# Performance work log

Measured on AMD Instinct MI355X. Metric: run time of the kernel, lower is better.

Reference implementation:

```python
import jax, jax.numpy as jnp
import numpy as np

NUM_LAYERS = 5  # shared parameters across layers


def _crelu(z):
    # complex ReLU: ReLU applied independently to real and imag parts
    return jnp.maximum(z.real, 0.0) + 1j * jnp.maximum(z.imag, 0.0)


def _layer(Habs2, diagH, noise, maxpow, v, ar, dl, rc):
    # ---- u step ----
    # cov: [B,K,1] = |H|^2 @ |v|^2 (sum over last dim keepdim is identity for width-1) + noise
    cov = jnp.sum(Habs2 @ (jnp.abs(v) ** 2), axis=-1, keepdims=True) + noise[..., None]
    u = diagH[..., None] * v / cov  # [B,K,1] complex
    # ---- w step ---- (w_poly=None branch)
    err = 1.0 - jnp.conj(u) * diagH[..., None] * v
    w = 1.0 / err  # [B,K,1] complex
    # ---- v step ----
    v_tilde = jnp.conj(diagH)[..., None] * u * w  # [B,K,1]
    ul = (jnp.abs(u) ** 2) * jnp.abs(w)  # real [B,K,1]
    ul = jnp.sum(jnp.abs(jnp.swapaxes(Habs2, -2, -1) @ ul), axis=-1, keepdims=True)
    mu = jnp.maximum(jnp.abs(v_tilde) / jnp.sqrt(maxpow)[..., None] - ul, 0.0)
    ula = (ul + mu).astype(v_tilde.dtype)
    # ar + diagload branches: [B,K,1,1] @ [1,C] -> [B,K,1,C]
    vt = (v_tilde / ula)[..., None] @ ar + v_tilde[..., None] @ dl
    # nonlin + recombination: [B,K,1,C] @ [C,1] -> [B,K,1,1]
    vt = _crelu(vt) @ rc
    v_new = vt[..., 0]  # [B,K,1]
    # power correction
    cur = jnp.maximum(maxpow[..., None], jnp.abs(v_new) ** 2)
    corr = jnp.minimum(jnp.sqrt(maxpow[..., None] / cur), 1.0)
    return v_new * corr, u, w


def setup_inputs() -> dict:
    key = jax.random.key(0)
    ks = jax.random.split(key, 12)
    B, K, C = 64, 512, 4
    s = 1.0 / np.sqrt(C + 1)
    inp = {
        "h_re": jax.random.normal(ks[0], (B, K, K), jnp.float32),
        "h_im": jax.random.normal(ks[1], (B, K, K), jnp.float32),
        "user_noise_pow": jax.random.uniform(ks[2], (B, K), jnp.float32, 0.1, 1.0),
        "bss_maxpow": jnp.ones((B, K), jnp.float32),
        "v_in_re": jax.random.normal(ks[3], (B, K, 1), jnp.float32) * 0.5,
        "v_in_im": jax.random.normal(ks[4], (B, K, 1), jnp.float32) * 0.5,
        "ar_re": jax.random.normal(ks[5], (1, C), jnp.float32) * s,
        "ar_im": jax.random.normal(ks[6], (1, C), jnp.float32) * s,
        "dl_re": jax.random.normal(ks[7], (1, C), jnp.float32) * s,
        "dl_im": jax.random.normal(ks[8], (1, C), jnp.float32) * s,
        "rc_re": jax.random.normal(ks[9], (C, 1), jnp.float32) * s,
        "rc_im": jax.random.normal(ks[10], (C, 1), jnp.float32) * s,
    }
    return inp


def reference(h_re, h_im, user_noise_pow, bss_maxpow, v_in_re, v_in_im,
              ar_re, ar_im, dl_re, dl_im, rc_re, rc_im):
    H = (h_re + 1j * h_im).astype(jnp.complex64)
    Habs2 = h_re * h_re + h_im * h_im  # |H|^2, real [B,K,K]
    diagH = jnp.diagonal(H, axis1=-2, axis2=-1)  # [B,K]
    v = (v_in_re + 1j * v_in_im).astype(jnp.complex64)
    ar = (ar_re + 1j * ar_im).astype(jnp.complex64)
    dl = (dl_re + 1j * dl_im).astype(jnp.complex64)
    rc = (rc_re + 1j * rc_im).astype(jnp.complex64)
    vs = []
    for _ in range(NUM_LAYERS):
        v, u, w = _layer(Habs2, diagH, user_noise_pow, bss_maxpow, v, ar, dl, rc)
        vs.append(v)
    vstack = jnp.stack(vs, 0)  # [L,B,K,1] complex
    # return real/imag stacked so the output is a real tensor: [L,B,K,1,2]
    return jnp.stack([vstack.real, vstack.imag], axis=-1)
```

## Files before the change

### kernel.cpp

```cpp
#include <hip/hip_runtime.h>

#define B    64
#define K    512
#define C    4
#define NL   5
#define BK   (B*K)
#define ROWS 128
#define NT   1024
#define GRID (B*4)

typedef _Float16 half_t;
typedef _Float16 half8 __attribute__((ext_vector_type(8)));
typedef float    f4    __attribute__((ext_vector_type(4)));

#define PART_OFF   0
#define VST_OFF    (36*K*4)
#define XSQ_OFF    (VST_OFF + K*8)
#define MPL_OFF    (XSQ_OFF + K*4)
#define NZ_OFF     (MPL_OFF + K*4)
#define DAB_OFF    (NZ_OFF + ROWS*4)
#define RSB_OFF    (DAB_OFF + ROWS*4)
#define SMEM_BYTES (RSB_OFF + ROWS*4)

__device__ __forceinline__ float ld_l3(const float* p) {
    return __uint_as_float(__hip_atomic_load((const unsigned*)p,
        __ATOMIC_RELAXED, __HIP_MEMORY_SCOPE_AGENT));
}
__device__ __forceinline__ void st_l3(float* p, float v) {
    __hip_atomic_store((unsigned*)p, __float_as_uint(v),
        __ATOMIC_RELAXED, __HIP_MEMORY_SCOPE_AGENT);
}
__device__ __forceinline__ void st_l3_2(float2* p, float2 v) {
    unsigned long long u = ((unsigned long long)__float_as_uint(v.y) << 32)
                         | (unsigned long long)__float_as_uint(v.x);
    __hip_atomic_store((unsigned long long*)p, u,
        __ATOMIC_RELAXED, __HIP_MEMORY_SCOPE_AGENT);
}
__device__ __forceinline__ float2 ld_l3_2(const float2* p) {
    unsigned long long u = __hip_atomic_load((const unsigned long long*)p,
        __ATOMIC_RELAXED, __HIP_MEMORY_SCOPE_AGENT);
    return make_float2(__uint_as_float((unsigned)(u & 0xffffffffu)),
                       __uint_as_float((unsigned)(u >> 32)));
}

__global__ __launch_bounds__(NT, 4) void k_all(
    const float* __restrict__ hre,  const float* __restrict__ him,
    const float* __restrict__ noise,const float* __restrict__ mp,
    const float* __restrict__ vre,  const float* __restrict__ vim,
    const float* __restrict__ ar_re,const float* __restrict__ ar_im,
    const float* __restrict__ dl_re,const float* __restrict__ dl_im,
    const float* __restrict__ rc_re,const float* __restrict__ rc_im,
    float2* __restrict__ vtilde,
    float*  __restrict__ ulpart,
    unsigned* __restrict__ bar,
    float* __restrict__ out)
{
    extern __shared__ char smem[];
    float*  part  = (float*) (smem + PART_OFF);
    float2* vst   = (float2*)(smem + VST_OFF);
    float*  xsq   = (float*) (smem + XSQ_OFF);
    float*  mpl   = (float*) (smem + MPL_OFF);
    float*  nz    = (float*) (smem + NZ_OFF);
    float*  dab   = (float*) (smem + DAB_OFF);
    float*  rsbuf = (float*) (smem + RSB_OFF);

    const int tid  = threadIdx.x;
    const int lane = tid & 63;
    const int w    = tid >> 6;
    const int b    = blockIdx.x & 63;
    const int q    = blockIdx.x >> 6;
    const int j0   = q * ROWS;
    unsigned* qb   = bar + ((unsigned)b << 5);

    if (tid < K) {
        float a = vre[b * K + tid], c2 = vim[b * K + tid];
        vst[tid] = make_float2(a, c2);
        xsq[tid] = a * a + c2 * c2;
        mpl[tid] = mp[b * K + tid];
    } else if (tid < K + ROWS) {
        nz[tid - K] = noise[b * K + j0 + (tid - K)];
    }
    __syncthreads();

    half8 h[8];
    {
        const f4 xa = ((const f4*)xsq)[lane * 2];
        const f4 xb = ((const f4*)xsq)[lane * 2 + 1];
        const size_t gb = ((size_t)b * K + j0) * K;
        const f4* rp = (const f4*)(hre + gb);
        const f4* ip = (const f4*)(him + gb);
        f4 lr0[2], lr1[2], li0[2], li1[2];
        lr0[0] = __builtin_nontemporal_load(rp + tid * 2);
        lr1[0] = __builtin_nontemporal_load(rp + tid * 2 + 1);
        li0[0] = __builtin_nontemporal_load(ip + tid * 2);
        li1[0] = __builtin_nontemporal_load(ip + tid * 2 + 1);
#pragma unroll
        for (int i = 0; i < 8; ++i) {
            const int cur = i & 1, nxt = cur ^ 1;
            if (i < 7) {
                const int e4 = (i + 1) * (NT * 2) + tid * 2;
                lr0[nxt] = __builtin_nontemporal_load(rp + e4);
                lr1[nxt] = __builtin_nontemporal_load(rp + e4 + 1);
                li0[nxt] = __builtin_nontemporal_load(ip + e4);
                li1[nxt] = __builtin_nontemporal_load(ip + e4 + 1);
            }
            const f4 r0 = lr0[cur], r1 = lr1[cur];
            const f4 m0 = li0[cur], m1 = li1[cur];
            float s[8];
            s[0] = r0.x*r0.x + m0.x*m0.x; s[1] = r0.y*r0.y + m0.y*m0.y;
            s[2] = r0.z*r0.z + m0.z*m0.z; s[3] = r0.w*r0.w + m0.w*m0.w;
            s[4] = r1.x*r1.x + m1.x*m1.x; s[5] = r1.y*r1.y + m1.y*m1.y;
            s[6] = r1.z*r1.z + m1.z*m1.z; s[7] = r1.w*r1.w + m1.w*m1.w;
            half8 hh;
#pragma unroll
            for (int t = 0; t < 8; ++t) hh[t] = (_Float16)s[t];
            h[i] = hh;
            const int row  = i * 16 + w;
            const int col0 = lane * 8;
            const int j    = j0 + row;
            if (j >= col0 && j < col0 + 8) dab[row] = s[j - col0];
            float acc = s[0]*xa.x + s[1]*xa.y + s[2]*xa.z + s[3]*xa.w +
                        s[4]*xb.x + s[5]*xb.y + s[6]*xb.z + s[7]*xb.w;
#pragma unroll
            for (int off = 32; off; off >>= 1) acc += __shfl_xor(acc, off, 64);
            if (lane == 0) rsbuf[row] = acc;
        }
    }

    for (int l = 0; l < NL; ++l) {
        const int buf = l & 1;
        if (l > 0) {
            const f4 xa = ((const f4*)xsq)[lane * 2];
            const f4 xb = ((const f4*)xsq)[lane * 2 + 1];
#pragma unroll
            for (int r = 0; r < 8; ++r) {
                float acc = (float)h[r][0]*xa.x + (float)h[r][1]*xa.y +
                            (float)h[r][2]*xa.z + (float)h[r][3]*xa.w +
                            (float)h[r][4]*xb.x + (float)h[r][5]*xb.y +
                            (float)h[r][6]*xb.z + (float)h[r][7]*xb.w;
#pragma unroll
                for (int off = 32; off; off >>= 1) acc += __shfl_xor(acc, off, 64);
                if (lane == 0) rsbuf[r * 16 + w] = acc;
            }
        }
        float ulv_own = 0.f;
        if (lane < 8) {
            const int row = 16 * lane + w;
            const int j   = j0 + row;
            const int bj  = b * K + j;
            const float cov = rsbuf[row] + nz[row];
            const float d2  = dab[row];
            const float A   = d2 * xsq[j];
            const float ww  = cov / (cov - A);
            const float sc  = d2 * ww / cov;
            const float2 vv = vst[j];
            st_l3_2(&vtilde[buf * BK + bj], make_float2(sc * vv.x, sc * vv.y));
            ulv_own = A * ww / (cov * cov);
        }
        float ulv[8];
#pragma unroll
        for (int r = 0; r < 8; ++r) ulv[r] = __shfl(ulv_own, r, 64);

        float pw[8];
#pragma unroll
        for (int t = 0; t < 8; ++t) {
            pw[t] = (float)h[0][t]*ulv[0] + (float)h[1][t]*ulv[1] +
                    (float)h[2][t]*ulv[2] + (float)h[3][t]*ulv[3] +
                    (float)h[4][t]*ulv[4] + (float)h[5][t]*ulv[5] +
                    (float)h[6][t]*ulv[6] + (float)h[7][t]*ulv[7];
        }
        float* pr = part + w * K + lane * 8;
#pragma unroll
        for (int t = 0; t < 8; ++t) pr[t] = pw[t];
        __syncthreads();

        float s2 = 0.f;
        if (tid < K) {
#pragma unroll
            for (int ws2 = 0; ws2 < 16; ++ws2) s2 += part[ws2 * K + tid];
            st_l3(&ulpart[(size_t)buf * (B*4*K) + ((size_t)(b*4 + q)) * K + tid],
                  s2);
        }
        __syncthreads();
        if (tid == 0)
            __hip_atomic_fetch_add(qb, 1u, __ATOMIC_RELAXED,
                                   __HIP_MEMORY_SCOPE_AGENT);
        if (lane == 0) {
            const unsigned target = 4u * (unsigned)(l + 1);
            while (__hip_atomic_load(qb, __ATOMIC_RELAXED,
                                     __HIP_MEMORY_SCOPE_AGENT) < target)
                __builtin_amdgcn_s_sleep(2);
        }
        asm volatile("" ::: "memory");

        if (tid < K) {
            const int k  = tid;
            const int bk = b * K + k;
            const float* up = ulpart + (size_t)buf * (B*4*K) + (size_t)(b*4) * K;
            const float2 vt = ld_l3_2(&vtilde[buf * BK + bk]);
            float ul = s2;
#pragma unroll
            for (int qq = 0; qq < 4; ++qq)
                if (qq != q) ul += ld_l3(up + qq * K + k);
            const float p   = mpl[k];
            const float avt = sqrtf(vt.x*vt.x + vt.y*vt.y);
            const float mu  = fmaxf(avt / sqrtf(p) - ul, 0.f);
            const float inv = 1.f / (ul + mu);
            float ax = 0.f, ay = 0.f;
#pragma unroll
            for (int c = 0; c < C; ++c) {
                const float gre = ar_re[c] * inv + dl_re[c];
                const float gim = ar_im[c] * inv + dl_im[c];
                float zre = vt.x * gre - vt.y * gim;
                float zim = vt.x * gim + vt.y * gre;
                zre = fmaxf(zre, 0.f);
                zim = fmaxf(zim, 0.f);
                ax += zre * rc_re[c] - zim * rc_im[c];
                ay += zre * rc_im[c] + zim * rc_re[c];
            }
            const float n2   = ax*ax + ay*ay;
            const float cur  = fmaxf(p, n2);
            const float corr = fminf(sqrtf(p / cur), 1.f);
            ax *= corr; ay *= corr;
            if ((k >> 7) == q)
                ((float2*)out)[(size_t)l * BK + bk] = make_float2(ax, ay);
            vst[k] = make_float2(ax, ay);
            xsq[k] = ax * ax + ay * ay;
        }
        __syncthreads();
    }
}

extern "C" void kernel_launch(void* const* d_in, const int* in_sizes, int n_in,
                              void* d_out, int out_size, void* d_ws, size_t ws_size,
                              hipStream_t stream) {
    const float* hre   = (const float*)d_in[0];
    const float* him   = (const float*)d_in[1];
    const float* noise = (const float*)d_in[2];
    const float* mp    = (const float*)d_in[3];
    const float* vre   = (const float*)d_in[4];
    const float* vim   = (const float*)d_in[5];
    const float* ar_re = (const float*)d_in[6];
    const float* ar_im = (const float*)d_in[7];
    const float* dl_re = (const float*)d_in[8];
    const float* dl_im = (const float*)d_in[9];
    const float* rc_re = (const float*)d_in[10];
    const float* rc_im = (const float*)d_in[11];
    float* out = (float*)d_out;

    char*     ws     = (char*)d_ws;
    float2*   vtilde = (float2*)ws;
    float*    ulpart = (float*)(ws + 2*(size_t)BK*8);
    unsigned* bar    = (unsigned*)(ws + 2*(size_t)BK*8 + 2*(size_t)B*4*K*4);

    static bool attr_done = false;
    if (!attr_done) {
        hipFuncSetAttribute((const void*)k_all,
                            hipFuncAttributeMaxDynamicSharedMemorySize,
                            SMEM_BYTES);
        attr_done = true;
    }

    hipMemsetAsync(bar, 0, B * 32 * sizeof(unsigned), stream);

    hipLaunchKernelGGL(k_all, dim3(GRID), dim3(NT), SMEM_BYTES, stream,
                       hre, him, noise, mp, vre, vim,
                       ar_re, ar_im, dl_re, dl_im, rc_re, rc_im,
                       vtilde, ulpart, bar, out);
}
```

Before: 188.6 us.

## Interleave column ownership per lane and use DPP wave reductions

Changes the per-lane column mapping from eight contiguous columns to a stride-64 interleave, so global loads become coalesced scalar loads and LDS accesses in the ul partial write become conflict-free. Replaces shuffle-based wave reductions with DPP row operations plus readlane, and keeps row sums in registers instead of an LDS buffer. The ulv broadcast uses readlane instead of shfl. The cost is 16 scalar nontemporal loads per row instead of 4 vector loads, which may raise instruction count on the bandwidth-bound load of H.

```diff
diff --git a/kernel.cpp b/kernel.cpp
--- a/kernel.cpp
+++ b/kernel.cpp
@@ -11,7 +11,6 @@
 
 typedef _Float16 half_t;
 typedef _Float16 half8 __attribute__((ext_vector_type(8)));
-typedef float    f4    __attribute__((ext_vector_type(4)));
 
 #define PART_OFF   0
 #define VST_OFF    (36*K*4)
@@ -19,8 +18,7 @@
 #define MPL_OFF    (XSQ_OFF + K*4)
 #define NZ_OFF     (MPL_OFF + K*4)
 #define DAB_OFF    (NZ_OFF + ROWS*4)
-#define RSB_OFF    (DAB_OFF + ROWS*4)
-#define SMEM_BYTES (RSB_OFF + ROWS*4)
+#define SMEM_BYTES (DAB_OFF + ROWS*4)
 
 __device__ __forceinline__ float ld_l3(const float* p) {
     return __uint_as_float(__hip_atomic_load((const unsigned*)p,
@@ -41,6 +39,22 @@
         __ATOMIC_RELAXED, __HIP_MEMORY_SCOPE_AGENT);
     return make_float2(__uint_as_float((unsigned)(u & 0xffffffffu)),
                        __uint_as_float((unsigned)(u >> 32)));
+}
+
+template <int CTRL, int ROWMASK>
+__device__ __forceinline__ float dppadd(float x) {
+    int t = __builtin_amdgcn_update_dpp(0, __float_as_int(x), CTRL, ROWMASK,
+                                        0xf, true);
+    return x + __int_as_float(t);
+}
+__device__ __forceinline__ float wsum(float x) {
+    x = dppadd<0x111, 0xf>(x);
+    x = dppadd<0x112, 0xf>(x);
+    x = dppadd<0x114, 0xf>(x);
+    x = dppadd<0x118, 0xf>(x);
+    x = dppadd<0x142, 0xa>(x);
+    x = dppadd<0x143, 0xc>(x);
+    return __int_as_float(__builtin_amdgcn_readlane(__float_as_int(x), 63));
 }
 
 __global__ __launch_bounds__(NT, 4) void k_all(
@@ -56,13 +70,12 @@
     float* __restrict__ out)
 {
     extern __shared__ char smem[];
-    float*  part  = (float*) (smem + PART_OFF);
-    float2* vst   = (float2*)(smem + VST_OFF);
-    float*  xsq   = (float*) (smem + XSQ_OFF);
-    float*  mpl   = (float*) (smem + MPL_OFF);
-    float*  nz    = (float*) (smem + NZ_OFF);
-    float*  dab   = (float*) (smem + DAB_OFF);
-    float*  rsbuf = (float*) (smem + RSB_OFF);
+    float*  part = (float*) (smem + PART_OFF);
+    float2* vst  = (float2*)(smem + VST_OFF);
+    float*  xsq  = (float*) (smem + XSQ_OFF);
+    float*  mpl  = (float*) (smem + MPL_OFF);
+    float*  nz   = (float*) (smem + NZ_OFF);
+    float*  dab  = (float*) (smem + DAB_OFF);
 
     const int tid  = threadIdx.x;
     const int lane = tid & 63;
@@ -82,73 +95,73 @@
     }
     __syncthreads();
 
+    float xq[8];
+#pragma unroll
+    for (int t = 0; t < 8; ++t) xq[t] = xsq[t * 64 + lane];
+
     half8 h[8];
+    float rs0[8];
     {
-        const f4 xa = ((const f4*)xsq)[lane * 2];
-        const f4 xb = ((const f4*)xsq)[lane * 2 + 1];
         const size_t gb = ((size_t)b * K + j0) * K;
-        const f4* rp = (const f4*)(hre + gb);
-        const f4* ip = (const f4*)(him + gb);
-        f4 lr0[2], lr1[2], li0[2], li1[2];
-        lr0[0] = __builtin_nontemporal_load(rp + tid * 2);
-        lr1[0] = __builtin_nontemporal_load(rp + tid * 2 + 1);
-        li0[0] = __builtin_nontemporal_load(ip + tid * 2);
-        li1[0] = __builtin_nontemporal_load(ip + tid * 2 + 1);
+        float ra[2][8], ia[2][8];
+#pragma unroll
+        for (int t = 0; t < 8; ++t) {
+            ra[0][t] = __builtin_nontemporal_load(hre + gb + (size_t)w * K + t * 64 + lane);
+            ia[0][t] = __builtin_nontemporal_load(him + gb + (size_t)w * K + t * 64 + lane);
+        }
 #pragma unroll
         for (int i = 0; i < 8; ++i) {
             const int cur = i & 1, nxt = cur ^ 1;
             if (i < 7) {
-                const int e4 = (i + 1) * (NT * 2) + tid * 2;
-                lr0[nxt] = __builtin_nontemporal_load(rp + e4);
-                lr1[nxt] = __builtin_nontemporal_load(rp + e4 + 1);
-                li0[nxt] = __builtin_nontemporal_load(ip + e4);
-                li1[nxt] = __builtin_nontemporal_load(ip + e4 + 1);
-            }
-            const f4 r0 = lr0[cur], r1 = lr1[cur];
-            const f4 m0 = li0[cur], m1 = li1[cur];
-            float s[8];
-            s[0] = r0.x*r0.x + m0.x*m0.x; s[1] = r0.y*r0.y + m0.y*m0.y;
-            s[2] = r0.z*r0.z + m0.z*m0.z; s[3] = r0.w*r0.w + m0.w*m0.w;
-            s[4] = r1.x*r1.x + m1.x*m1.x; s[5] = r1.y*r1.y + m1.y*m1.y;
-            s[6] = r1.z*r1.z + m1.z*m1.z; s[7] = r1.w*r1.w + m1.w*m1.w;
+                const size_t rb = gb + (size_t)(16 * (i + 1) + w) * K;
+#pragma unroll
+                for (int t = 0; t < 8; ++t) {
+                    ra[nxt][t] = __builtin_nontemporal_load(hre + rb + t * 64 + lane);
+                    ia[nxt][t] = __builtin_nontemporal_load(him + rb + t * 64 + lane);
+                }
+            }
+            float s[8], acc = 0.f;
             half8 hh;
 #pragma unroll
-            for (int t = 0; t < 8; ++t) hh[t] = (_Float16)s[t];
+            for (int t = 0; t < 8; ++t) {
+                s[t]  = ra[cur][t] * ra[cur][t] + ia[cur][t] * ia[cur][t];
+                hh[t] = (_Float16)s[t];
+                acc  += s[t] * xq[t];
+            }
             h[i] = hh;
-            const int row  = i * 16 + w;
-            const int col0 = lane * 8;
-            const int j    = j0 + row;
-            if (j >= col0 && j < col0 + 8) dab[row] = s[j - col0];
-            float acc = s[0]*xa.x + s[1]*xa.y + s[2]*xa.z + s[3]*xa.w +
-                        s[4]*xb.x + s[5]*xb.y + s[6]*xb.z + s[7]*xb.w;
-#pragma unroll
-            for (int off = 32; off; off >>= 1) acc += __shfl_xor(acc, off, 64);
-            if (lane == 0) rsbuf[row] = acc;
+            const int row = 16 * i + w;
+            const int j   = j0 + row;
+            if (lane == (j & 63)) dab[row] = s[j >> 6];
+            rs0[i] = wsum(acc);
         }
     }
 
     for (int l = 0; l < NL; ++l) {
         const int buf = l & 1;
-        if (l > 0) {
-            const f4 xa = ((const f4*)xsq)[lane * 2];
-            const f4 xb = ((const f4*)xsq)[lane * 2 + 1];
+        float scov[8];
+        if (l == 0) {
+#pragma unroll
+            for (int r = 0; r < 8; ++r) scov[r] = rs0[r];
+        } else {
+#pragma unroll
+            for (int t = 0; t < 8; ++t) xq[t] = xsq[t * 64 + lane];
 #pragma unroll
             for (int r = 0; r < 8; ++r) {
-                float acc = (float)h[r][0]*xa.x + (float)h[r][1]*xa.y +
-                            (float)h[r][2]*xa.z + (float)h[r][3]*xa.w +
-                            (float)h[r][4]*xb.x + (float)h[r][5]*xb.y +
-                            (float)h[r][6]*xb.z + (float)h[r][7]*xb.w;
-#pragma unroll
-                for (int off = 32; off; off >>= 1) acc += __shfl_xor(acc, off, 64);
-                if (lane == 0) rsbuf[r * 16 + w] = acc;
+                float acc = 0.f;
+#pragma unroll
+                for (int t = 0; t < 8; ++t) acc += (float)h[r][t] * xq[t];
+                scov[r] = wsum(acc);
             }
         }
         float ulv_own = 0.f;
         if (lane < 8) {
+            float s = scov[0];
+#pragma unroll
+            for (int r = 1; r < 8; ++r) s = (lane == r) ? scov[r] : s;
             const int row = 16 * lane + w;
             const int j   = j0 + row;
             const int bj  = b * K + j;
-            const float cov = rsbuf[row] + nz[row];
+            const float cov = s + nz[row];
             const float d2  = dab[row];
             const float A   = d2 * xsq[j];
             const float ww  = cov / (cov - A);
@@ -159,19 +172,17 @@
         }
         float ulv[8];
 #pragma unroll
-        for (int r = 0; r < 8; ++r) ulv[r] = __shfl(ulv_own, r, 64);
-
-        float pw[8];
+        for (int r = 0; r < 8; ++r)
+            ulv[r] = __int_as_float(
+                __builtin_amdgcn_readlane(__float_as_int(ulv_own), r));
+
 #pragma unroll
         for (int t = 0; t < 8; ++t) {
-            pw[t] = (float)h[0][t]*ulv[0] + (float)h[1][t]*ulv[1] +
-                    (float)h[2][t]*ulv[2] + (float)h[3][t]*ulv[3] +
-                    (float)h[4][t]*ulv[4] + (float)h[5][t]*ulv[5] +
-                    (float)h[6][t]*ulv[6] + (float)h[7][t]*ulv[7];
-        }
-        float* pr = part + w * K + lane * 8;
-#pragma unroll
-        for (int t = 0; t < 8; ++t) pr[t] = pw[t];
+            float a = 0.f;
+#pragma unroll
+            for (int r = 0; r < 8; ++r) a += (float)h[r][t] * ulv[r];
+            part[w * K + t * 64 + lane] = a;
+        }
         __syncthreads();
 
         float s2 = 0.f;
@@ -255,13 +266,13 @@
 
     static bool attr_done = false;
     if (!attr_done) {
-        hipFuncSetAttribute((const void*)k_all,
-                            hipFuncAttributeMaxDynamicSharedMemorySize,
-                            SMEM_BYTES);
+        (void)hipFuncSetAttribute((const void*)k_all,
+                                  hipFuncAttributeMaxDynamicSharedMemorySize,
+                                  SMEM_BYTES);
         attr_done = true;
     }
 
-    hipMemsetAsync(bar, 0, B * 32 * sizeof(unsigned), stream);
+    (void)hipMemsetAsync(bar, 0, B * 32 * sizeof(unsigned), stream);
 
     hipLaunchKernelGGL(k_all, dim3(GRID), dim3(NT), SMEM_BYTES, stream,
                        hre, him, noise, mp, vre, vim,
```

Result: no change. 189.6 us (+0.5%).
